# Performance work log

Hardware: AMD Instinct MI355X
Metric: run time of the kernel (lower is better)

The kernel has to match this reference:

```python
import jax, jax.numpy as jnp
import numpy as np

N_NODES = 10000
N_FEATS = 128
BSZ = 32
D = 100000


def setup_inputs() -> dict:
    key = jax.random.key(0)
    k_vals, k_idx = jax.random.split(key)
    flat_inputs = jax.random.normal(k_vals, (BSZ, D), dtype=jnp.float32)
    # Sample D UNIQUE (node, feat) slots per batch row so the scatter has no
    # duplicate destinations (torch duplicate writes are nondeterministic).
    n_slots = N_NODES * N_FEATS
    keys = jax.random.split(k_idx, BSZ)
    flat_pos = jax.vmap(lambda k: jax.random.permutation(k, n_slots)[:D])(keys)  # [BSZ, D]
    node_ids = (flat_pos // N_FEATS).astype(jnp.int64)
    feat_ids = (flat_pos % N_FEATS).astype(jnp.int64)
    return {"flat_inputs": flat_inputs, "node_ids": node_ids, "feat_ids": feat_ids}


def reference(flat_inputs, node_ids, feat_ids):
    bsz, d = flat_inputs.shape
    # Linearize (batch, node, feat) -> single flat index; one fused scatter.
    batch_ids = jnp.arange(bsz, dtype=node_ids.dtype)[:, None]  # [bsz, 1] broadcasts over D
    lin = (batch_ids * N_NODES + node_ids) * N_FEATS + feat_ids  # [bsz, D]
    obs_mat = jnp.zeros((bsz * N_NODES * N_FEATS,), dtype=flat_inputs.dtype)
    obs_mat = obs_mat.at[lin.reshape(-1)].set(flat_inputs.reshape(-1), unique_indices=True)
    return obs_mat.reshape(bsz, N_NODES, N_FEATS)
```

## Files before the change

### kernel.cpp

```cpp
#include <hip/hip_runtime.h>
#include <stdint.h>

#define N_NODES 10000
#define N_FEATS 128
#define BSZ 32
#define D_ELEMS 100000

#define OUT_ELEMS (BSZ * N_NODES * N_FEATS)
#define N_ITEMS   (BSZ * D_ELEMS)
#define N_GROUPS  (N_ITEMS / 4)

#define NBUCKET 512
#define CHUNK   (OUT_ELEMS / NBUCKET)
#define CAP     8064
#define SUBF    16000
#define NSUB    (CHUNK / SUBF)

#define BIN_GPB   1024
#define BIN_IPB   (BIN_GPB * 4)
#define BIN_NBLK  ((N_GROUPS + BIN_GPB - 1) / BIN_GPB)

typedef float f32x4 __attribute__((ext_vector_type(4)));
typedef int   i32x4 __attribute__((ext_vector_type(4)));

__global__ __launch_bounds__(512) void bin_kernel(
    const f32x4* __restrict__ vals,
    const i32x4* __restrict__ nodes,
    const i32x4* __restrict__ feats,
    uint64_t* __restrict__ pairs,
    uint32_t* __restrict__ gcount) {
  __shared__ uint32_t hist[NBUCKET];
  __shared__ uint32_t excl[NBUCKET];
  __shared__ uint32_t base_s[NBUCKET];
  __shared__ uint32_t wpart[8];
  __shared__ uint32_t tot_s;
  __shared__ alignas(16) uint64_t sp[BIN_IPB];
  const int tid = threadIdx.x;
  hist[tid] = 0;
  __syncthreads();

  uint32_t lin[8]; float val[8]; uint32_t rnk[8];
  const int gbase = blockIdx.x * BIN_GPB;
#pragma unroll
  for (int q = 0; q < 2; ++q) {
    int g = gbase + q * 512 + tid;
    bool a = (g < N_GROUPS);
    int gg = a ? g : 0;
    f32x4 v = vals[gg];
    i32x4 n = nodes[gg];
    i32x4 f = feats[gg];
    uint32_t rowbase = (uint32_t)((gg * 4) / D_ELEMS) * (uint32_t)(N_NODES * N_FEATS);
    lin[q*4+0] = a ? rowbase + (uint32_t)n.x * N_FEATS + (uint32_t)f.x : 0xFFFFFFFFu;
    lin[q*4+1] = a ? rowbase + (uint32_t)n.y * N_FEATS + (uint32_t)f.y : 0xFFFFFFFFu;
    lin[q*4+2] = a ? rowbase + (uint32_t)n.z * N_FEATS + (uint32_t)f.z : 0xFFFFFFFFu;
    lin[q*4+3] = a ? rowbase + (uint32_t)n.w * N_FEATS + (uint32_t)f.w : 0xFFFFFFFFu;
    val[q*4+0] = v.x; val[q*4+1] = v.y; val[q*4+2] = v.z; val[q*4+3] = v.w;
  }

#pragma unroll
  for (int i = 0; i < 8; ++i)
    if (lin[i] != 0xFFFFFFFFu)
      rnk[i] = atomicAdd(&hist[lin[i] / CHUNK], 1u);
  __syncthreads();

  uint32_t h = hist[tid];
  uint32_t v = h;
#pragma unroll
  for (int s = 1; s < 64; s <<= 1) {
    uint32_t u = __shfl_up(v, s, 64);
    if ((tid & 63) >= s) v += u;
  }
  if ((tid & 63) == 63) wpart[tid >> 6] = v;
  __syncthreads();
  if (tid < 64) {
    uint32_t p = (tid < 8) ? wpart[tid] : 0u;
#pragma unroll
    for (int s = 1; s < 8; s <<= 1) {
      uint32_t u = __shfl_up(p, s, 64);
      if (tid >= s) p += u;
    }
    if (tid < 8) wpart[tid] = p;
  }
  __syncthreads();
  uint32_t woff = (tid >= 64) ? wpart[(tid >> 6) - 1] : 0u;
  uint32_t incl = v + woff;
  excl[tid] = incl - h;
  base_s[tid] = h ? atomicAdd(&gcount[tid], h) : 0u;
  if (tid == 511) tot_s = incl;
  __syncthreads();

#pragma unroll
  for (int i = 0; i < 8; ++i) {
    if (lin[i] != 0xFFFFFFFFu) {
      uint32_t b = lin[i] / CHUNK;
      sp[excl[b] + rnk[i]] =
          ((uint64_t)__float_as_uint(val[i]) << 32) | (uint64_t)lin[i];
    }
  }
  __syncthreads();

  const uint32_t tot = tot_s;
  for (uint32_t i = tid; i < tot; i += 512u) {
    uint64_t p = sp[i];
    uint32_t l = (uint32_t)p;
    uint32_t b = l / CHUNK;
    uint32_t dst = base_s[b] + (i - excl[b]);
    if (dst < CAP) pairs[(size_t)b * CAP + dst] = p;
  }
}

__global__ __launch_bounds__(1024) void expand_kernel(
    const uint64_t* __restrict__ pairs,
    const uint32_t* __restrict__ gcount,
    float* __restrict__ out) {
  __shared__ float chunk[SUBF];
  const int b = blockIdx.x;
  const int tid = threadIdx.x;
  uint32_t cnt = gcount[b];
  if (cnt > CAP) cnt = CAP;

  uint32_t ml[8];
  float    mv[8];
  const uint64_t* bp = pairs + (size_t)b * CAP;
  const uint32_t cbase = (uint32_t)(b * CHUNK);
#pragma unroll
  for (int i = 0; i < 8; ++i) {
    uint32_t idx = (uint32_t)tid + (uint32_t)i * 1024u;
    uint64_t p = (idx < cnt) ? bp[idx] : ~0ull;
    ml[i] = (uint32_t)p - cbase;
    mv[i] = __uint_as_float((uint32_t)(p >> 32));
  }

  f32x4* c4 = (f32x4*)chunk;
  const f32x4 z = {0.f, 0.f, 0.f, 0.f};
#pragma unroll
  for (int j = 0; j < 4; ++j) {
    int idx = tid + j * 1024;
    if (idx < SUBF / 4) c4[idx] = z;
  }
  __syncthreads();

  const size_t outbase = (size_t)b * CHUNK;
  for (int p = 0; p < NSUB; ++p) {
    uint32_t lo = (uint32_t)(p * SUBF);
#pragma unroll
    for (int i = 0; i < 8; ++i) {
      uint32_t loc = ml[i] - lo;
      if (loc < SUBF) chunk[loc] = mv[i];
    }
    __syncthreads();
    f32x4* o4 = (f32x4*)(out + outbase + lo);
#pragma unroll
    for (int j = 0; j < 4; ++j) {
      int idx = tid + j * 1024;
      if (idx < SUBF / 4) {
        f32x4 v = c4[idx];
        c4[idx] = z;
        o4[idx] = v;
      }
    }
    __syncthreads();
  }
}

__global__ __launch_bounds__(256) void scatter4_kernel(
    const f32x4* __restrict__ vals,
    const i32x4* __restrict__ node_ids,
    const i32x4* __restrict__ feat_ids,
    float* __restrict__ out) {
  int t = blockIdx.x * blockDim.x + threadIdx.x;
  if (t >= N_GROUPS) return;
  int b = (t * 4) / D_ELEMS;
  f32x4 v = vals[t];
  i32x4 n = node_ids[t];
  i32x4 f = feat_ids[t];
  size_t base = (size_t)b * N_NODES * N_FEATS;
  out[base + (size_t)n.x * N_FEATS + (size_t)f.x] = v.x;
  out[base + (size_t)n.y * N_FEATS + (size_t)f.y] = v.y;
  out[base + (size_t)n.z * N_FEATS + (size_t)f.z] = v.z;
  out[base + (size_t)n.w * N_FEATS + (size_t)f.w] = v.w;
}

extern "C" void kernel_launch(void* const* d_in, const int* in_sizes, int n_in,
                              void* d_out, int out_size, void* d_ws, size_t ws_size,
                              hipStream_t stream) {
  const float* vals     = (const float*)d_in[0];
  const int*   node_ids = (const int*)d_in[1];
  const int*   feat_ids = (const int*)d_in[2];
  float* out = (float*)d_out;

  const size_t pairs_bytes = (size_t)NBUCKET * CAP * sizeof(uint64_t);
  const size_t need = pairs_bytes + NBUCKET * sizeof(uint32_t);

  if (ws_size >= need) {
    uint64_t* pairs  = (uint64_t*)d_ws;
    uint32_t* gcount = (uint32_t*)((char*)d_ws + pairs_bytes);
    hipMemsetAsync(gcount, 0, NBUCKET * sizeof(uint32_t), stream);
    bin_kernel<<<BIN_NBLK, 512, 0, stream>>>(
        (const f32x4*)vals, (const i32x4*)node_ids, (const i32x4*)feat_ids,
        pairs, gcount);
    expand_kernel<<<NBUCKET, 1024, 0, stream>>>(pairs, gcount, out);
  } else {
    hipMemsetAsync(out, 0, (size_t)out_size * sizeof(float), stream);
    const int grid = (N_GROUPS + 255) / 256;
    scatter4_kernel<<<grid, 256, 0, stream>>>(
        (const f32x4*)vals, (const i32x4*)node_ids, (const i32x4*)feat_ids, out);
  }
}
```

Baseline: 49.01 us.

## Fuse binning and expansion into one cooperative kernel with grid syncs

```diff
diff --git a/kernel.cpp b/kernel.cpp
--- a/kernel.cpp
+++ b/kernel.cpp
@@ -1,5 +1,8 @@
 #include <hip/hip_runtime.h>
+#include <hip/hip_cooperative_groups.h>
 #include <stdint.h>
+
+namespace cg = cooperative_groups;
 
 #define N_NODES 10000
 #define N_FEATS 128
@@ -13,15 +16,174 @@
 #define NBUCKET 512
 #define CHUNK   (OUT_ELEMS / NBUCKET)
 #define CAP     8064
-#define SUBF    16000
+#define SUBF    8000
 #define NSUB    (CHUNK / SUBF)
 
+#define FGPB  ((N_GROUPS + NBUCKET - 1) / NBUCKET)
+#define SP_N  6272
+
 #define BIN_GPB   1024
-#define BIN_IPB   (BIN_GPB * 4)
 #define BIN_NBLK  ((N_GROUPS + BIN_GPB - 1) / BIN_GPB)
 
 typedef float f32x4 __attribute__((ext_vector_type(4)));
 typedef int   i32x4 __attribute__((ext_vector_type(4)));
+
+__global__ __launch_bounds__(1024, 2) void fused_kernel(
+    const f32x4* __restrict__ vals,
+    const i32x4* __restrict__ nodes,
+    const i32x4* __restrict__ feats,
+    uint64_t* __restrict__ pairs,
+    uint32_t* __restrict__ gcount,
+    float* __restrict__ out) {
+  __shared__ alignas(16) uint8_t smem[64512];
+  uint64_t* sp     = (uint64_t*)smem;
+  uint32_t* hist   = (uint32_t*)(smem + 50176);
+  uint32_t* excl   = (uint32_t*)(smem + 52224);
+  uint32_t* base_s = (uint32_t*)(smem + 54272);
+  uint32_t* wpart  = (uint32_t*)(smem + 56320);
+  uint32_t* tot_p  = (uint32_t*)(smem + 56384);
+
+  cg::grid_group grid = cg::this_grid();
+  const int tid = threadIdx.x;
+  const int blk = blockIdx.x;
+
+  if (tid == 0) gcount[blk] = 0u;
+  if (tid < NBUCKET) hist[tid] = 0u;
+  __syncthreads();
+
+  uint32_t lin[8]; float val[8]; uint32_t rnk[8];
+  const int gbase = blk * FGPB;
+#pragma unroll
+  for (int q = 0; q < 2; ++q) {
+    int sub = q * 1024 + tid;
+    int g = gbase + sub;
+    bool a = (sub < FGPB) && (g < N_GROUPS);
+    int gg = a ? g : 0;
+    f32x4 v = vals[gg];
+    i32x4 n = nodes[gg];
+    i32x4 f = feats[gg];
+    uint32_t rowbase = (uint32_t)((gg * 4) / D_ELEMS) * (uint32_t)(N_NODES * N_FEATS);
+    lin[q*4+0] = a ? rowbase + (uint32_t)n.x * N_FEATS + (uint32_t)f.x : 0xFFFFFFFFu;
+    lin[q*4+1] = a ? rowbase + (uint32_t)n.y * N_FEATS + (uint32_t)f.y : 0xFFFFFFFFu;
+    lin[q*4+2] = a ? rowbase + (uint32_t)n.z * N_FEATS + (uint32_t)f.z : 0xFFFFFFFFu;
+    lin[q*4+3] = a ? rowbase + (uint32_t)n.w * N_FEATS + (uint32_t)f.w : 0xFFFFFFFFu;
+    val[q*4+0] = v.x; val[q*4+1] = v.y; val[q*4+2] = v.z; val[q*4+3] = v.w;
+  }
+
+#pragma unroll
+  for (int i = 0; i < 8; ++i)
+    if (lin[i] != 0xFFFFFFFFu)
+      rnk[i] = atomicAdd(&hist[lin[i] / CHUNK], 1u);
+  __syncthreads();
+
+  uint32_t h = 0, v = 0;
+  if (tid < NBUCKET) {
+    h = hist[tid];
+    v = h;
+#pragma unroll
+    for (int s = 1; s < 64; s <<= 1) {
+      uint32_t u = __shfl_up(v, s, 64);
+      if ((tid & 63) >= s) v += u;
+    }
+    if ((tid & 63) == 63) wpart[tid >> 6] = v;
+  }
+  __syncthreads();
+  if (tid < 64) {
+    uint32_t p = (tid < 8) ? wpart[tid] : 0u;
+#pragma unroll
+    for (int s = 1; s < 8; s <<= 1) {
+      uint32_t u = __shfl_up(p, s, 64);
+      if (tid >= s) p += u;
+    }
+    if (tid < 8) wpart[tid] = p;
+  }
+  __syncthreads();
+  if (tid < NBUCKET) {
+    uint32_t woff = (tid >= 64) ? wpart[(tid >> 6) - 1] : 0u;
+    uint32_t incl = v + woff;
+    excl[tid] = incl - h;
+    if (tid == NBUCKET - 1) *tot_p = incl;
+  }
+  __syncthreads();
+
+#pragma unroll
+  for (int i = 0; i < 8; ++i) {
+    if (lin[i] != 0xFFFFFFFFu) {
+      uint32_t b = lin[i] / CHUNK;
+      sp[excl[b] + rnk[i]] =
+          ((uint64_t)__float_as_uint(val[i]) << 32) | (uint64_t)lin[i];
+    }
+  }
+  const uint32_t tot = *tot_p;
+
+  grid.sync();
+
+  if (tid < NBUCKET)
+    base_s[tid] = h ? atomicAdd(&gcount[tid], h) : 0u;
+  __syncthreads();
+  for (uint32_t i = tid; i < tot; i += 1024u) {
+    uint64_t p = sp[i];
+    uint32_t l = (uint32_t)p;
+    uint32_t b = l / CHUNK;
+    uint32_t dst = base_s[b] + (i - excl[b]);
+    if (dst < CAP) pairs[(size_t)b * CAP + dst] = p;
+  }
+
+  grid.sync();
+
+  uint32_t cnt = gcount[blk];
+  if (cnt > CAP) cnt = CAP;
+  uint32_t ml[8]; float mv[8];
+  const uint64_t* bp = pairs + (size_t)blk * CAP;
+  const uint32_t cbase = (uint32_t)(blk * CHUNK);
+#pragma unroll
+  for (int i = 0; i < 8; ++i) {
+    uint32_t idx = (uint32_t)tid + (uint32_t)i * 1024u;
+    uint64_t p = (idx < cnt) ? bp[idx] : ~0ull;
+    ml[i] = (uint32_t)p - cbase;
+    mv[i] = __uint_as_float((uint32_t)(p >> 32));
+  }
+
+  float* chunk = (float*)smem;
+  f32x4* c4 = (f32x4*)chunk;
+  const f32x4 z = {0.f, 0.f, 0.f, 0.f};
+#pragma unroll
+  for (int j = 0; j < 4; ++j) {
+    int idx = tid + j * 1024;
+    if (idx < (2 * SUBF) / 4) c4[idx] = z;
+  }
+  __syncthreads();
+
+#pragma unroll
+  for (int i = 0; i < 8; ++i)
+    if (ml[i] < SUBF) chunk[ml[i]] = mv[i];
+  __syncthreads();
+
+  const size_t outbase = (size_t)blk * CHUNK;
+  for (int p = 0; p < NSUB; ++p) {
+    if (p + 1 < NSUB) {
+      uint32_t lo = (uint32_t)((p + 1) * SUBF);
+      float* dsth = chunk + ((p + 1) & 1) * SUBF;
+#pragma unroll
+      for (int i = 0; i < 8; ++i) {
+        uint32_t loc = ml[i] - lo;
+        if (loc < SUBF) dsth[loc] = mv[i];
+      }
+    }
+    f32x4* src = (f32x4*)(chunk + (p & 1) * SUBF);
+    f32x4* o4  = (f32x4*)(out + outbase + (size_t)p * SUBF);
+#pragma unroll
+    for (int j = 0; j < 2; ++j) {
+      int idx = tid + j * 1024;
+      if (idx < SUBF / 4) {
+        f32x4 w = src[idx];
+        src[idx] = z;
+        o4[idx] = w;
+      }
+    }
+    __syncthreads();
+  }
+}
 
 __global__ __launch_bounds__(512) void bin_kernel(
     const f32x4* __restrict__ vals,
@@ -34,7 +196,7 @@
   __shared__ uint32_t base_s[NBUCKET];
   __shared__ uint32_t wpart[8];
   __shared__ uint32_t tot_s;
-  __shared__ alignas(16) uint64_t sp[BIN_IPB];
+  __shared__ alignas(16) uint64_t sp[BIN_GPB * 4];
   const int tid = threadIdx.x;
   hist[tid] = 0;
   __syncthreads();
@@ -113,14 +275,13 @@
     const uint64_t* __restrict__ pairs,
     const uint32_t* __restrict__ gcount,
     float* __restrict__ out) {
-  __shared__ float chunk[SUBF];
+  __shared__ alignas(16) float chunk[2 * SUBF];
   const int b = blockIdx.x;
   const int tid = threadIdx.x;
   uint32_t cnt = gcount[b];
   if (cnt > CAP) cnt = CAP;
 
-  uint32_t ml[8];
-  float    mv[8];
+  uint32_t ml[8]; float mv[8];
   const uint64_t* bp = pairs + (size_t)b * CAP;
   const uint32_t cbase = (uint32_t)(b * CHUNK);
 #pragma unroll
@@ -136,27 +297,35 @@
 #pragma unroll
   for (int j = 0; j < 4; ++j) {
     int idx = tid + j * 1024;
-    if (idx < SUBF / 4) c4[idx] = z;
-  }
+    if (idx < (2 * SUBF) / 4) c4[idx] = z;
+  }
+  __syncthreads();
+
+#pragma unroll
+  for (int i = 0; i < 8; ++i)
+    if (ml[i] < SUBF) chunk[ml[i]] = mv[i];
   __syncthreads();
 
   const size_t outbase = (size_t)b * CHUNK;
   for (int p = 0; p < NSUB; ++p) {
-    uint32_t lo = (uint32_t)(p * SUBF);
-#pragma unroll
-    for (int i = 0; i < 8; ++i) {
-      uint32_t loc = ml[i] - lo;
-      if (loc < SUBF) chunk[loc] = mv[i];
-    }
-    __syncthreads();
-    f32x4* o4 = (f32x4*)(out + outbase + lo);
-#pragma unroll
-    for (int j = 0; j < 4; ++j) {
+    if (p + 1 < NSUB) {
+      uint32_t lo = (uint32_t)((p + 1) * SUBF);
+      float* dsth = chunk + ((p + 1) & 1) * SUBF;
+#pragma unroll
+      for (int i = 0; i < 8; ++i) {
+        uint32_t loc = ml[i] - lo;
+        if (loc < SUBF) dsth[loc] = mv[i];
+      }
+    }
+    f32x4* src = (f32x4*)(chunk + (p & 1) * SUBF);
+    f32x4* o4  = (f32x4*)(out + outbase + (size_t)p * SUBF);
+#pragma unroll
+    for (int j = 0; j < 2; ++j) {
       int idx = tid + j * 1024;
       if (idx < SUBF / 4) {
-        f32x4 v = c4[idx];
-        c4[idx] = z;
-        o4[idx] = v;
+        f32x4 w = src[idx];
+        src[idx] = z;
+        o4[idx] = w;
       }
     }
     __syncthreads();
@@ -184,9 +353,9 @@
 extern "C" void kernel_launch(void* const* d_in, const int* in_sizes, int n_in,
                               void* d_out, int out_size, void* d_ws, size_t ws_size,
                               hipStream_t stream) {
-  const float* vals     = (const float*)d_in[0];
-  const int*   node_ids = (const int*)d_in[1];
-  const int*   feat_ids = (const int*)d_in[2];
+  const f32x4* vals  = (const f32x4*)d_in[0];
+  const i32x4* nodes = (const i32x4*)d_in[1];
+  const i32x4* feats = (const i32x4*)d_in[2];
   float* out = (float*)d_out;
 
   const size_t pairs_bytes = (size_t)NBUCKET * CAP * sizeof(uint64_t);
@@ -195,15 +364,20 @@
   if (ws_size >= need) {
     uint64_t* pairs  = (uint64_t*)d_ws;
     uint32_t* gcount = (uint32_t*)((char*)d_ws + pairs_bytes);
+
+    void* kargs[] = {(void*)&vals, (void*)&nodes, (void*)&feats,
+                     (void*)&pairs, (void*)&gcount, (void*)&out};
+    hipError_t e = hipLaunchCooperativeKernel(
+        (void*)fused_kernel, dim3(NBUCKET), dim3(1024), kargs, 0, stream);
+    if (e == hipSuccess) return;
+    (void)hipGetLastError();
+
     hipMemsetAsync(gcount, 0, NBUCKET * sizeof(uint32_t), stream);
-    bin_kernel<<<BIN_NBLK, 512, 0, stream>>>(
-        (const f32x4*)vals, (const i32x4*)node_ids, (const i32x4*)feat_ids,
-        pairs, gcount);
+    bin_kernel<<<BIN_NBLK, 512, 0, stream>>>(vals, nodes, feats, pairs, gcount);
     expand_kernel<<<NBUCKET, 1024, 0, stream>>>(pairs, gcount, out);
   } else {
     hipMemsetAsync(out, 0, (size_t)out_size * sizeof(float), stream);
     const int grid = (N_GROUPS + 255) / 256;
-    scatter4_kernel<<<grid, 256, 0, stream>>>(
-        (const f32x4*)vals, (const i32x4*)node_ids, (const i32x4*)feat_ids, out);
-  }
-}
+    scatter4_kernel<<<grid, 256, 0, stream>>>(vals, nodes, feats, out);
+  }
+}
```

After: 143.8 us. +193.4%, slower.
